# Performance work log

Hardware: AMD Instinct MI355X
Metric: run time of the kernel (lower is better)

The kernel has to match this reference:

```python
import jax, jax.numpy as jnp
import numpy as np

COST_CLASS = 1.0
COST_MASK = 1.0
COST_DICE = 1.0


def setup_inputs() -> dict:
    key = jax.random.key(0)
    k1, k2, k3, k4 = jax.random.split(key, 4)
    B, Q, G, T, L = 16, 100, 16384, 50, 21
    masks_queries_logits = jax.random.normal(k1, (B, Q, G), dtype=jnp.float32)
    class_queries_logits = jax.random.normal(k2, (B, Q, L), dtype=jnp.float32)
    mask_labels = (jax.random.uniform(k3, (B, T, G)) < 0.1).astype(jnp.float32)
    class_labels = jax.random.randint(k4, (B, T), 0, L, dtype=jnp.int64)
    return {
        "masks_queries_logits": masks_queries_logits,
        "class_queries_logits": class_queries_logits,
        "mask_labels": mask_labels,
        "class_labels": class_labels,
    }


def reference(masks_queries_logits, class_queries_logits, mask_labels, class_labels):
    """Returns the [B, Q, T] Hungarian cost matrices (the GPU-side compute of the
    matcher). The scipy linear_sum_assignment step is CPU-side and excluded."""
    G = masks_queries_logits.shape[-1]
    L = class_queries_logits.shape[-1]

    # classification cost: -softmax(pred)[:, target_class]
    probs = jax.nn.softmax(class_queries_logits, axis=-1)          # [B,Q,L]
    onehot = jax.nn.one_hot(class_labels, L, dtype=probs.dtype)    # [B,T,L]
    cost_class = -jnp.einsum('bql,btl->bqt', probs, onehot)        # [B,Q,T]

    # pairwise sigmoid cross-entropy cost (BCE-with-logits vs target 1 / target 0)
    ce_pos = jax.nn.softplus(-masks_queries_logits)                # [B,Q,G]
    ce_neg = jax.nn.softplus(masks_queries_logits)                 # [B,Q,G]
    cost_mask = (jnp.einsum('bqg,btg->bqt', ce_pos, mask_labels)
                 + jnp.einsum('bqg,btg->bqt', ce_neg, 1.0 - mask_labels)) / G

    # pairwise dice cost
    sig = jax.nn.sigmoid(masks_queries_logits)                     # [B,Q,G]
    numerator = 2.0 * jnp.einsum('bqg,btg->bqt', sig, mask_labels)
    denominator = sig.sum(-1)[:, :, None] + mask_labels.sum(-1)[:, None, :]
    cost_dice = 1.0 - (numerator + 1.0) / (denominator + 1.0)

    return COST_MASK * cost_mask + COST_CLASS * cost_class + COST_DICE * cost_dice
```

## Files before the change

### kernel.cpp

```cpp
#include <hip/hip_runtime.h>
#include <stdint.h>

#define NB 16
#define NQ 100
#define QP 112
#define NG 16384
#define NT 50
#define TP 64
#define NL 21
#define GW 512

#define OFF_BITS  0u
#define SZ_BITS   (NB*TP*GW*4u)
#define OFF_MSUM  (OFF_BITS + SZ_BITS)
#define SZ_MSUM   (NB*TP*4u)
#define OFF_SSP   (OFF_MSUM + SZ_MSUM)
#define SZ_SSP    (NB*QP*4u)
#define OFF_SSG   (OFF_SSP + SZ_SSP)
#define OFF_DOTM  (OFF_SSG + SZ_SSP)
#define SZ_DOT    (NB*QP*TP*4u)
#define OFF_DOTS  (OFF_DOTM + SZ_DOT)
#define ZERO_OFF  OFF_SSP
#define ZERO_SZ   (SZ_SSP*2u + SZ_DOT*2u)

typedef __bf16 bf16x8 __attribute__((ext_vector_type(8)));
typedef float f32x4 __attribute__((ext_vector_type(4)));
union Frag { uint32_t u[4]; bf16x8 v; };

__device__ __forceinline__ uint32_t pack_bf16(float a, float b) {
  uint32_t ua = __float_as_uint(a), ub = __float_as_uint(b);
  ua = (ua + 0x7FFFu + ((ua >> 16) & 1u)) >> 16;
  ub = (ub + 0x7FFFu + ((ub >> 16) & 1u)) & 0xFFFF0000u;
  return ua | ub;
}

__global__ __launch_bounds__(256) void pack_kernel(
    const float* __restrict__ mask, uint32_t* __restrict__ bits,
    float* __restrict__ msum) {
  int blk = blockIdx.x;
  int b = blk >> 6, t = blk & 63;
  int tid = threadIdx.x;
  int lane = tid & 63, wv = tid >> 6;
  uint32_t* wrow = bits + (size_t)(b*TP + t) * GW;
  if (t < NT) {
    const float* src = mask + (size_t)(b*NT + t) * NG;
    __shared__ int partial[4];
    int cnt = 0;
    int wbase = wv * 4096;
    for (int it = 0; it < 64; ++it) {
      int gb = wbase + it * 64;
      float v = src[gb + lane];
      unsigned long long bal = __ballot(v > 0.5f);
      if (lane == 0) wrow[gb >> 5] = (uint32_t)bal;
      if (lane == 1) wrow[(gb >> 5) + 1] = (uint32_t)(bal >> 32);
      cnt += (int)__popcll(bal);
    }
    if (lane == 0) partial[wv] = cnt;
    __syncthreads();
    if (tid == 0)
      msum[b*TP + t] = (float)(partial[0] + partial[1] + partial[2] + partial[3]);
  } else {
    for (int i = tid; i < GW; i += 256) wrow[i] = 0u;
    if (tid == 0) msum[b*TP + t] = 0.f;
  }
}

__global__ __launch_bounds__(448) void main_kernel(
    const float* __restrict__ m, const uint32_t* __restrict__ bits,
    float* __restrict__ ssp, float* __restrict__ ssg,
    float* __restrict__ dotm, float* __restrict__ dotsg) {
  int b = blockIdx.x >> 4;
  int chunk = blockIdx.x & 15;
  int tid = threadIdx.x;
  int wv = tid >> 6, lane = tid & 63;
  int row16 = lane & 15, lg = lane >> 4;

  __shared__ uint32_t lbits[TP][33];
  for (int i = tid; i < TP * 32; i += 448) {
    int t = i >> 5, k = i & 31;
    lbits[t][k] = bits[(size_t)(b*TP + t) * GW + chunk*32 + k];
  }
  __syncthreads();

  int q0 = wv * 16;
  int qrow = q0 + row16; if (qrow > NQ - 1) qrow = NQ - 1;
  const float* arow = m + (size_t)(b*NQ + qrow) * NG + chunk*1024 + lg*8;

  f32x4 accm[4], accs[4];
#pragma unroll
  for (int nt = 0; nt < 4; ++nt) {
    accm[nt] = (f32x4)(0.f);
    accs[nt] = (f32x4)(0.f);
  }
  float sspacc = 0.f, ssgacc = 0.f;

  for (int ks = 0; ks < 32; ++ks) {
    const float4* p = (const float4*)(arow + ks*32);
    float4 v0 = p[0], v1 = p[1];
    float av[8] = {v0.x, v0.y, v0.z, v0.w, v1.x, v1.y, v1.z, v1.w};
    Frag mf, sf;
#pragma unroll
    for (int j = 0; j < 8; j += 2) {
      float x0 = av[j], x1 = av[j+1];
      float e0 = __expf(-fabsf(x0)), e1 = __expf(-fabsf(x1));
      float r0 = __builtin_amdgcn_rcpf(1.f + e0);
      float r1 = __builtin_amdgcn_rcpf(1.f + e1);
      float sg0 = (x0 >= 0.f) ? r0 : 1.f - r0;
      float sg1 = (x1 >= 0.f) ? r1 : 1.f - r1;
      float sp0 = fmaxf(x0, 0.f) + __logf(1.f + e0);
      float sp1 = fmaxf(x1, 0.f) + __logf(1.f + e1);
      sspacc += sp0 + sp1;
      ssgacc += sg0 + sg1;
      mf.u[j >> 1] = pack_bf16(x0, x1);
      sf.u[j >> 1] = pack_bf16(sg0, sg1);
    }
#pragma unroll
    for (int nt = 0; nt < 4; ++nt) {
      int t = nt*16 + row16;
      uint32_t w = lbits[t][ks];
      uint32_t byte = (w >> (lg * 8)) & 0xFFu;
      Frag bf;
#pragma unroll
      for (int j = 0; j < 4; ++j) {
        uint32_t lo = (byte >> (2*j)) & 1u, hi = (byte >> (2*j + 1)) & 1u;
        bf.u[j] = (lo ? 0x3F80u : 0u) | (hi ? 0x3F800000u : 0u);
      }
      accm[nt] = __builtin_amdgcn_mfma_f32_16x16x32_bf16(mf.v, bf.v, accm[nt], 0, 0, 0);
      accs[nt] = __builtin_amdgcn_mfma_f32_16x16x32_bf16(sf.v, bf.v, accs[nt], 0, 0, 0);
    }
  }

  sspacc += __shfl_xor(sspacc, 16); sspacc += __shfl_xor(sspacc, 32);
  ssgacc += __shfl_xor(ssgacc, 16); ssgacc += __shfl_xor(ssgacc, 32);
  if (lg == 0) {
    atomicAdd(&ssp[b*QP + q0 + row16], sspacc);
    atomicAdd(&ssg[b*QP + q0 + row16], ssgacc);
  }
#pragma unroll
  for (int nt = 0; nt < 4; ++nt) {
    int t = nt*16 + row16;
#pragma unroll
    for (int r = 0; r < 4; ++r) {
      int qq = q0 + lg*4 + r;
      atomicAdd(&dotm[(size_t)(b*QP + qq)*TP + t], accm[nt][r]);
      atomicAdd(&dotsg[(size_t)(b*QP + qq)*TP + t], accs[nt][r]);
    }
  }
}

__global__ __launch_bounds__(64) void finalize_kernel(
    const float* __restrict__ cls, const int* __restrict__ labels,
    const float* __restrict__ msum, const float* __restrict__ ssp,
    const float* __restrict__ ssg, const float* __restrict__ dotm,
    const float* __restrict__ dotsg, float* __restrict__ out) {
  int blk = blockIdx.x;
  int b = blk / NQ, q = blk % NQ;
  int lane = threadIdx.x;
  const float* lgt = cls + (size_t)(b*NQ + q) * NL;
  float v = (lane < NL) ? lgt[lane] : -1e30f;
  float mx = v;
  for (int s = 32; s; s >>= 1) mx = fmaxf(mx, __shfl_xor(mx, s));
  float e = (lane < NL) ? __expf(v - mx) : 0.f;
  float se = e;
  for (int s = 32; s; s >>= 1) se += __shfl_xor(se, s);

  if (lane < NT) {
    int lbl = labels[b*NT + lane];
    float p = __expf(lgt[lbl] - mx) / se;
    float s1 = ssp[b*QP + q];
    float sg = ssg[b*QP + q];
    float dm = dotm[(size_t)(b*QP + q)*TP + lane];
    float ds = dotsg[(size_t)(b*QP + q)*TP + lane];
    float cmask = (s1 - dm) * (1.f / (float)NG);
    float cdice = 1.f - (2.f*ds + 1.f) / (sg + msum[b*TP + lane] + 1.f);
    out[(size_t)(b*NQ + q)*NT + lane] = cmask - p + cdice;
  }
}

extern "C" void kernel_launch(void* const* d_in, const int* in_sizes, int n_in,
                              void* d_out, int out_size, void* d_ws, size_t ws_size,
                              hipStream_t stream) {
  const float* mq = (const float*)d_in[0];
  const float* cq = (const float*)d_in[1];
  const float* ml = (const float*)d_in[2];
  const int*   cl = (const int*)d_in[3];
  char* ws = (char*)d_ws;
  uint32_t* bits = (uint32_t*)(ws + OFF_BITS);
  float* msum = (float*)(ws + OFF_MSUM);
  float* ssp  = (float*)(ws + OFF_SSP);
  float* ssg  = (float*)(ws + OFF_SSG);
  float* dotm = (float*)(ws + OFF_DOTM);
  float* dotsg= (float*)(ws + OFF_DOTS);

  hipMemsetAsync(ws + ZERO_OFF, 0, ZERO_SZ, stream);
  pack_kernel<<<NB*TP, 256, 0, stream>>>(ml, bits, msum);
  main_kernel<<<NB*16, 448, 0, stream>>>(mq, bits, ssp, ssg, dotm, dotsg);
  finalize_kernel<<<NB*NQ, 64, 0, stream>>>(cq, cl, msum, ssp, ssg, dotm, dotsg, (float*)d_out);
}
```

Before: 249.7 us.

## Pre-pack mask labels as bf16 MFMA fragments and fold row sums into GEMM

Adds a v2 path, taken when the workspace is large enough. Target masks are pre-packed as bf16 tiles already in MFMA B-fragment layout, so the main kernel loads fragments directly instead of expanding bits in LDS. An all-ones padding target (t=63) makes the MFMA produce the per-query sum of sigmoid and logit. Softplus is rewritten algebraically as x + log(1+e^-x), which removes the abs/select work and the separate sigmoid-sum accumulator. The main kernel now runs many small 64-thread blocks over 512-point chunks. In exchange it writes and reads a 32 MB packed buffer instead of a 2 MB bitmask, and the unguarded exp(-x) may overflow for very negative logits.

```diff
diff --git a/kernel.cpp b/kernel.cpp
--- a/kernel.cpp
+++ b/kernel.cpp
@@ -10,19 +10,6 @@
 #define NL 21
 #define GW 512
 
-#define OFF_BITS  0u
-#define SZ_BITS   (NB*TP*GW*4u)
-#define OFF_MSUM  (OFF_BITS + SZ_BITS)
-#define SZ_MSUM   (NB*TP*4u)
-#define OFF_SSP   (OFF_MSUM + SZ_MSUM)
-#define SZ_SSP    (NB*QP*4u)
-#define OFF_SSG   (OFF_SSP + SZ_SSP)
-#define OFF_DOTM  (OFF_SSG + SZ_SSP)
-#define SZ_DOT    (NB*QP*TP*4u)
-#define OFF_DOTS  (OFF_DOTM + SZ_DOT)
-#define ZERO_OFF  OFF_SSP
-#define ZERO_SZ   (SZ_SSP*2u + SZ_DOT*2u)
-
 typedef __bf16 bf16x8 __attribute__((ext_vector_type(8)));
 typedef float f32x4 __attribute__((ext_vector_type(4)));
 union Frag { uint32_t u[4]; bf16x8 v; };
@@ -34,7 +21,156 @@
   return ua | ub;
 }
 
-__global__ __launch_bounds__(256) void pack_kernel(
+#define SZ_BP     ((size_t)NB*512*64*32*2)
+#define OFF_MSUM2 (SZ_BP)
+#define OFF_SSP2  (OFF_MSUM2 + NB*TP*4)
+#define OFF_DOTM2 (OFF_SSP2 + NB*QP*4)
+#define OFF_DOTS2 (OFF_DOTM2 + (size_t)NB*QP*TP*4)
+#define NEED_V2   (OFF_DOTS2 + (size_t)NB*QP*TP*4)
+#define ZERO2_OFF OFF_MSUM2
+#define ZERO2_SZ  (NEED_V2 - OFF_MSUM2)
+
+__global__ __launch_bounds__(64) void pack_v2(
+    const float* __restrict__ mask, uint32_t* __restrict__ bp,
+    float* __restrict__ msum) {
+  int blk = blockIdx.x;
+  int qtr = blk & 3, t = (blk >> 2) & 63, b = blk >> 8;
+  int lane = threadIdx.x;
+  uint32_t* dst = bp + (size_t)b * (512*64*16);
+  if (t < NT) {
+    const float* src = mask + ((size_t)(b*NT + t)) * NG + qtr*4096;
+    float cnt = 0.f;
+#pragma unroll 4
+    for (int it = 0; it < 16; ++it) {
+      int g = it*256 + lane*4;
+      float4 v = *(const float4*)(src + g);
+      cnt += v.x + v.y + v.z + v.w;
+      int gg = qtr*4096 + g;
+      uint32_t* w = dst + ((size_t)(gg >> 5) * 64 + t) * 16 + ((gg & 31) >> 1);
+      uint2 pk; pk.x = pack_bf16(v.x, v.y); pk.y = pack_bf16(v.z, v.w);
+      *(uint2*)w = pk;
+    }
+    cnt += __shfl_xor(cnt, 1);  cnt += __shfl_xor(cnt, 2);
+    cnt += __shfl_xor(cnt, 4);  cnt += __shfl_xor(cnt, 8);
+    cnt += __shfl_xor(cnt, 16); cnt += __shfl_xor(cnt, 32);
+    if (lane == 0) atomicAdd(&msum[b*TP + t], cnt);
+  } else {
+    uint32_t val = (t == 63) ? 0x3F803F80u : 0u;
+    for (int it = 0; it < 16; ++it) {
+      int gg = qtr*4096 + it*256 + lane*4;
+      uint32_t* w = dst + ((size_t)(gg >> 5) * 64 + t) * 16 + ((gg & 31) >> 1);
+      uint2 pk; pk.x = val; pk.y = val;
+      *(uint2*)w = pk;
+    }
+  }
+}
+
+__global__ __launch_bounds__(64) void main_v2(
+    const float* __restrict__ m, const char* __restrict__ bp,
+    float* __restrict__ ssp, float* __restrict__ dotm,
+    float* __restrict__ dotsg) {
+  int blk = blockIdx.x;
+  int chunk = blk & 31;
+  int qt = (blk >> 5) % 7;
+  int b = blk / 224;
+  int lane = threadIdx.x;
+  int row16 = lane & 15, lg = lane >> 4;
+  int q0 = qt * 16;
+  int qrow = q0 + row16; if (qrow > NQ-1) qrow = NQ-1;
+  const float* arow = m + (size_t)(b*NQ + qrow)*NG + chunk*512 + lg*8;
+  const char* bbase = bp + (size_t)b*2097152 + (size_t)chunk*65536
+                         + (row16*32 + lg*8)*2;
+
+  f32x4 accm[4], accs[4];
+#pragma unroll
+  for (int nt = 0; nt < 4; ++nt) { accm[nt] = (f32x4)(0.f); accs[nt] = (f32x4)(0.f); }
+  float sl = 0.f;
+
+#pragma unroll 2
+  for (int ks = 0; ks < 16; ++ks) {
+    const float4* p = (const float4*)(arow + ks*32);
+    float4 v0 = p[0], v1 = p[1];
+    float av[8] = {v0.x, v0.y, v0.z, v0.w, v1.x, v1.y, v1.z, v1.w};
+    Frag mf, sf;
+#pragma unroll
+    for (int j = 0; j < 8; j += 2) {
+      float x0 = av[j], x1 = av[j+1];
+      float e0 = __builtin_amdgcn_exp2f(x0 * -1.442695041f);
+      float e1 = __builtin_amdgcn_exp2f(x1 * -1.442695041f);
+      float u0 = 1.f + e0, u1 = 1.f + e1;
+      float r0 = __builtin_amdgcn_rcpf(u0), r1 = __builtin_amdgcn_rcpf(u1);
+      sl += __builtin_amdgcn_logf(u0) + __builtin_amdgcn_logf(u1);
+      mf.u[j >> 1] = pack_bf16(x0, x1);
+      sf.u[j >> 1] = pack_bf16(r0, r1);
+    }
+    const char* bk = bbase + ks*4096;
+#pragma unroll
+    for (int nt = 0; nt < 4; ++nt) {
+      bf16x8 bfrag = *(const bf16x8*)(bk + nt*1024);
+      accm[nt] = __builtin_amdgcn_mfma_f32_16x16x32_bf16(mf.v, bfrag, accm[nt], 0, 0, 0);
+      accs[nt] = __builtin_amdgcn_mfma_f32_16x16x32_bf16(sf.v, bfrag, accs[nt], 0, 0, 0);
+    }
+  }
+
+  sl += __shfl_xor(sl, 16); sl += __shfl_xor(sl, 32);
+  if (lg == 0) atomicAdd(&ssp[b*QP + q0 + row16], sl);
+
+#pragma unroll
+  for (int nt = 0; nt < 4; ++nt) {
+    int t = nt*16 + row16;
+#pragma unroll
+    for (int r = 0; r < 4; ++r) {
+      int qq = q0 + lg*4 + r;
+      atomicAdd(&dotm [(size_t)(b*QP + qq)*TP + t], accm[nt][r]);
+      atomicAdd(&dotsg[(size_t)(b*QP + qq)*TP + t], accs[nt][r]);
+    }
+  }
+}
+
+__global__ __launch_bounds__(64) void finalize_v2(
+    const float* __restrict__ cls, const int* __restrict__ labels,
+    const float* __restrict__ msum, const float* __restrict__ ssp,
+    const float* __restrict__ dotm, const float* __restrict__ dotsg,
+    float* __restrict__ out) {
+  int blk = blockIdx.x;
+  int b = blk / NQ, q = blk % NQ;
+  int lane = threadIdx.x;
+  const float* lgt = cls + (size_t)(b*NQ + q) * NL;
+  float v = (lane < NL) ? lgt[lane] : -1e30f;
+  float mx = v;
+  for (int s = 32; s; s >>= 1) mx = fmaxf(mx, __shfl_xor(mx, s));
+  float e = (lane < NL) ? __expf(v - mx) : 0.f;
+  float se = e;
+  for (int s = 32; s; s >>= 1) se += __shfl_xor(se, s);
+
+  if (lane < NT) {
+    int lbl = labels[b*NT + lane];
+    float p = __expf(lgt[lbl] - mx) / se;
+    size_t base = (size_t)(b*QP + q) * TP;
+    float s1 = dotm[base + 63] + 0.69314718056f * ssp[b*QP + q];
+    float sg = dotsg[base + 63];
+    float dm = dotm[base + lane];
+    float ds = dotsg[base + lane];
+    float cmask = (s1 - dm) * (1.f / (float)NG);
+    float cdice = 1.f - (2.f*ds + 1.f) / (sg + msum[b*TP + lane] + 1.f);
+    out[(size_t)(b*NQ + q)*NT + lane] = cmask - p + cdice;
+  }
+}
+
+#define OFF1_BITS  0u
+#define SZ1_BITS   (NB*TP*GW*4u)
+#define OFF1_MSUM  (OFF1_BITS + SZ1_BITS)
+#define SZ1_MSUM   (NB*TP*4u)
+#define OFF1_SSP   (OFF1_MSUM + SZ1_MSUM)
+#define SZ1_SSP    (NB*QP*4u)
+#define OFF1_SSG   (OFF1_SSP + SZ1_SSP)
+#define OFF1_DOTM  (OFF1_SSG + SZ1_SSP)
+#define SZ1_DOT    (NB*QP*TP*4u)
+#define OFF1_DOTS  (OFF1_DOTM + SZ1_DOT)
+#define ZERO1_OFF  OFF1_SSP
+#define ZERO1_SZ   (SZ1_SSP*2u + SZ1_DOT*2u)
+
+__global__ __launch_bounds__(256) void pack_v1(
     const float* __restrict__ mask, uint32_t* __restrict__ bits,
     float* __restrict__ msum) {
   int blk = blockIdx.x;
@@ -65,7 +201,7 @@
   }
 }
 
-__global__ __launch_bounds__(448) void main_kernel(
+__global__ __launch_bounds__(448) void main_v1(
     const float* __restrict__ m, const uint32_t* __restrict__ bits,
     float* __restrict__ ssp, float* __restrict__ ssg,
     float* __restrict__ dotm, float* __restrict__ dotsg) {
@@ -88,10 +224,7 @@
 
   f32x4 accm[4], accs[4];
 #pragma unroll
-  for (int nt = 0; nt < 4; ++nt) {
-    accm[nt] = (f32x4)(0.f);
-    accs[nt] = (f32x4)(0.f);
-  }
+  for (int nt = 0; nt < 4; ++nt) { accm[nt] = (f32x4)(0.f); accs[nt] = (f32x4)(0.f); }
   float sspacc = 0.f, ssgacc = 0.f;
 
   for (int ks = 0; ks < 32; ++ks) {
@@ -148,7 +281,7 @@
   }
 }
 
-__global__ __launch_bounds__(64) void finalize_kernel(
+__global__ __launch_bounds__(64) void finalize_v1(
     const float* __restrict__ cls, const int* __restrict__ labels,
     const float* __restrict__ msum, const float* __restrict__ ssp,
     const float* __restrict__ ssg, const float* __restrict__ dotm,
@@ -185,15 +318,27 @@
   const float* ml = (const float*)d_in[2];
   const int*   cl = (const int*)d_in[3];
   char* ws = (char*)d_ws;
-  uint32_t* bits = (uint32_t*)(ws + OFF_BITS);
-  float* msum = (float*)(ws + OFF_MSUM);
-  float* ssp  = (float*)(ws + OFF_SSP);
-  float* ssg  = (float*)(ws + OFF_SSG);
-  float* dotm = (float*)(ws + OFF_DOTM);
-  float* dotsg= (float*)(ws + OFF_DOTS);
-
-  hipMemsetAsync(ws + ZERO_OFF, 0, ZERO_SZ, stream);
-  pack_kernel<<<NB*TP, 256, 0, stream>>>(ml, bits, msum);
-  main_kernel<<<NB*16, 448, 0, stream>>>(mq, bits, ssp, ssg, dotm, dotsg);
-  finalize_kernel<<<NB*NQ, 64, 0, stream>>>(cq, cl, msum, ssp, ssg, dotm, dotsg, (float*)d_out);
-}
+
+  if (ws_size >= NEED_V2) {
+    uint32_t* bp  = (uint32_t*)(ws);
+    float* msum = (float*)(ws + OFF_MSUM2);
+    float* ssp  = (float*)(ws + OFF_SSP2);
+    float* dotm = (float*)(ws + OFF_DOTM2);
+    float* dotsg= (float*)(ws + OFF_DOTS2);
+    hipMemsetAsync(ws + ZERO2_OFF, 0, ZERO2_SZ, stream);
+    pack_v2<<<NB*64*4, 64, 0, stream>>>(ml, bp, msum);
+    main_v2<<<NB*7*32, 64, 0, stream>>>(mq, (const char*)bp, ssp, dotm, dotsg);
+    finalize_v2<<<NB*NQ, 64, 0, stream>>>(cq, cl, msum, ssp, dotm, dotsg, (float*)d_out);
+  } else {
+    uint32_t* bits = (uint32_t*)(ws + OFF1_BITS);
+    float* msum = (float*)(ws + OFF1_MSUM);
+    float* ssp  = (float*)(ws + OFF1_SSP);
+    float* ssg  = (float*)(ws + OFF1_SSG);
+    float* dotm = (float*)(ws + OFF1_DOTM);
+    float* dotsg= (float*)(ws + OFF1_DOTS);
+    hipMemsetAsync(ws + ZERO1_OFF, 0, ZERO1_SZ, stream);
+    pack_v1<<<NB*TP, 256, 0, stream>>>(ml, bits, msum);
+    main_v1<<<NB*16, 448, 0, stream>>>(mq, bits, ssp, ssg, dotm, dotsg);
+    finalize_v1<<<NB*NQ, 64, 0, stream>>>(cq, cl, msum, ssp, ssg, dotm, dotsg, (float*)d_out);
+  }
+}
```

Measured after the change: 226.2 us. -9.4%, faster.

## Fuse mask packing into main kernel and fold row sums into MFMA

Applied to the files above, without the earlier changes.

Removes the separate bit-packing kernel: each block now loads its mask slice directly as bf16 into shared memory, laid out in MFMA fragment order. An all-ones padding target column and a padding query row let the MFMAs produce the sigmoid and logit row sums and the mask column sums, so the separate reductions go away. Softplus is rewritten as log(1+exp(-x)) summed with a log2 intrinsic, and the grid moves to 1024 blocks with smaller G chunks. This trades an extra kernel launch and a packed-bits round trip for more atomics and reading the full fp32 masks per block, and the unclamped exp can overflow for very negative logits.

```diff
diff --git a/kernel.cpp b/kernel.cpp
--- a/kernel.cpp
+++ b/kernel.cpp
@@ -8,20 +8,15 @@
 #define NT 50
 #define TP 64
 #define NL 21
-#define GW 512
+#define CH 256
+#define NCHUNK (NG/CH)
 
-#define OFF_BITS  0u
-#define SZ_BITS   (NB*TP*GW*4u)
-#define OFF_MSUM  (OFF_BITS + SZ_BITS)
-#define SZ_MSUM   (NB*TP*4u)
-#define OFF_SSP   (OFF_MSUM + SZ_MSUM)
-#define SZ_SSP    (NB*QP*4u)
-#define OFF_SSG   (OFF_SSP + SZ_SSP)
-#define OFF_DOTM  (OFF_SSG + SZ_SSP)
-#define SZ_DOT    (NB*QP*TP*4u)
-#define OFF_DOTS  (OFF_DOTM + SZ_DOT)
-#define ZERO_OFF  OFF_SSP
-#define ZERO_SZ   (SZ_SSP*2u + SZ_DOT*2u)
+#define OFF_SSP  0u
+#define SZ_SSP   (NB*QP*4u)
+#define OFF_DOTM (OFF_SSP + SZ_SSP)
+#define SZ_DOT   ((size_t)NB*QP*TP*4u)
+#define OFF_DOTS (OFF_DOTM + SZ_DOT)
+#define ZERO_SZ  (OFF_DOTS + SZ_DOT)
 
 typedef __bf16 bf16x8 __attribute__((ext_vector_type(8)));
 typedef float f32x4 __attribute__((ext_vector_type(4)));
@@ -34,67 +29,66 @@
   return ua | ub;
 }
 
-__global__ __launch_bounds__(256) void pack_kernel(
-    const float* __restrict__ mask, uint32_t* __restrict__ bits,
-    float* __restrict__ msum) {
-  int blk = blockIdx.x;
-  int b = blk >> 6, t = blk & 63;
-  int tid = threadIdx.x;
-  int lane = tid & 63, wv = tid >> 6;
-  uint32_t* wrow = bits + (size_t)(b*TP + t) * GW;
-  if (t < NT) {
-    const float* src = mask + (size_t)(b*NT + t) * NG;
-    __shared__ int partial[4];
-    int cnt = 0;
-    int wbase = wv * 4096;
-    for (int it = 0; it < 64; ++it) {
-      int gb = wbase + it * 64;
-      float v = src[gb + lane];
-      unsigned long long bal = __ballot(v > 0.5f);
-      if (lane == 0) wrow[gb >> 5] = (uint32_t)bal;
-      if (lane == 1) wrow[(gb >> 5) + 1] = (uint32_t)(bal >> 32);
-      cnt += (int)__popcll(bal);
-    }
-    if (lane == 0) partial[wv] = cnt;
-    __syncthreads();
-    if (tid == 0)
-      msum[b*TP + t] = (float)(partial[0] + partial[1] + partial[2] + partial[3]);
-  } else {
-    for (int i = tid; i < GW; i += 256) wrow[i] = 0u;
-    if (tid == 0) msum[b*TP + t] = 0.f;
-  }
+__device__ __forceinline__ uint32_t cvtpk(float a, float b) {
+  uint32_t r;
+  asm("v_cvt_pk_bf16_f32 %0, %1, %2" : "=v"(r) : "v"(a), "v"(b));
+  return r;
 }
 
-__global__ __launch_bounds__(448) void main_kernel(
-    const float* __restrict__ m, const uint32_t* __restrict__ bits,
-    float* __restrict__ ssp, float* __restrict__ ssg,
-    float* __restrict__ dotm, float* __restrict__ dotsg) {
-  int b = blockIdx.x >> 4;
-  int chunk = blockIdx.x & 15;
+__global__ __launch_bounds__(448, 7) void fused_main(
+    const float* __restrict__ m, const float* __restrict__ mask,
+    float* __restrict__ ssp, float* __restrict__ dotm,
+    float* __restrict__ dots) {
+  __shared__ __align__(16) uint32_t bfr[8 * 4 * 64 * 4];
+  int blk = blockIdx.x;
+  int chunk = blk & (NCHUNK - 1), b = blk >> 6;
   int tid = threadIdx.x;
-  int wv = tid >> 6, lane = tid & 63;
-  int row16 = lane & 15, lg = lane >> 4;
 
-  __shared__ uint32_t lbits[TP][33];
-  for (int i = tid; i < TP * 32; i += 448) {
-    int t = i >> 5, k = i & 31;
-    lbits[t][k] = bits[(size_t)(b*TP + t) * GW + chunk*32 + k];
+  {
+    int sub = tid & 7, tb = tid >> 3;
+    uint2* U2 = (uint2*)bfr;
+    int half = sub & 1;
+    int lgs = sub >> 1;
+    for (int t = tb; t < 64; t += 56) {
+      int nt = t >> 4;
+      int l = lgs * 16 + (t & 15);
+      if (t < NT) {
+        const float* src = mask + ((size_t)(b*NT + t))*NG + chunk*CH + sub*4;
+#pragma unroll
+        for (int i = 0; i < 8; ++i) {
+          float4 f = *(const float4*)(src + i*32);
+          uint2 pk;
+          pk.x = pack_bf16(f.x, f.y);
+          pk.y = pack_bf16(f.z, f.w);
+          U2[((i*4 + nt)*64 + l)*2 + half] = pk;
+        }
+      } else {
+        uint32_t c = (t == 63) ? 0x3F803F80u : 0u;
+        uint2 pk; pk.x = c; pk.y = c;
+#pragma unroll
+        for (int i = 0; i < 8; ++i)
+          U2[((i*4 + nt)*64 + l)*2 + half] = pk;
+      }
+    }
   }
   __syncthreads();
 
+  int lane = tid & 63, wv = tid >> 6;
+  int row16 = lane & 15, lg = lane >> 4;
   int q0 = wv * 16;
-  int qrow = q0 + row16; if (qrow > NQ - 1) qrow = NQ - 1;
-  const float* arow = m + (size_t)(b*NQ + qrow) * NG + chunk*1024 + lg*8;
+  int qrow = q0 + row16;
+  bool pad = qrow > NQ - 1;
+  int qc = pad ? NQ - 1 : qrow;
+  const float* arow = m + (size_t)(b*NQ + qc)*NG + chunk*CH + lg*8;
+  const bf16x8* BF = (const bf16x8*)bfr;
 
   f32x4 accm[4], accs[4];
 #pragma unroll
-  for (int nt = 0; nt < 4; ++nt) {
-    accm[nt] = (f32x4)(0.f);
-    accs[nt] = (f32x4)(0.f);
-  }
-  float sspacc = 0.f, ssgacc = 0.f;
+  for (int nt = 0; nt < 4; ++nt) { accm[nt] = (f32x4)(0.f); accs[nt] = (f32x4)(0.f); }
+  float sl = 0.f;
 
-  for (int ks = 0; ks < 32; ++ks) {
+#pragma unroll 2
+  for (int ks = 0; ks < 8; ++ks) {
     const float4* p = (const float4*)(arow + ks*32);
     float4 v0 = p[0], v1 = p[1];
     float av[8] = {v0.x, v0.y, v0.z, v0.w, v1.x, v1.y, v1.z, v1.w};
@@ -102,40 +96,27 @@
 #pragma unroll
     for (int j = 0; j < 8; j += 2) {
       float x0 = av[j], x1 = av[j+1];
-      float e0 = __expf(-fabsf(x0)), e1 = __expf(-fabsf(x1));
-      float r0 = __builtin_amdgcn_rcpf(1.f + e0);
-      float r1 = __builtin_amdgcn_rcpf(1.f + e1);
-      float sg0 = (x0 >= 0.f) ? r0 : 1.f - r0;
-      float sg1 = (x1 >= 0.f) ? r1 : 1.f - r1;
-      float sp0 = fmaxf(x0, 0.f) + __logf(1.f + e0);
-      float sp1 = fmaxf(x1, 0.f) + __logf(1.f + e1);
-      sspacc += sp0 + sp1;
-      ssgacc += sg0 + sg1;
-      mf.u[j >> 1] = pack_bf16(x0, x1);
-      sf.u[j >> 1] = pack_bf16(sg0, sg1);
+      x0 = pad ? 1.f : x0;
+      x1 = pad ? 1.f : x1;
+      float e0 = __builtin_amdgcn_exp2f(x0 * -1.442695041f);
+      float e1 = __builtin_amdgcn_exp2f(x1 * -1.442695041f);
+      float u0 = 1.f + e0, u1 = 1.f + e1;
+      float r0 = __builtin_amdgcn_rcpf(u0), r1 = __builtin_amdgcn_rcpf(u1);
+      sl += __builtin_amdgcn_logf(u0) + __builtin_amdgcn_logf(u1);
+      mf.u[j >> 1] = cvtpk(x0, x1);
+      sf.u[j >> 1] = cvtpk(r0, r1);
     }
 #pragma unroll
     for (int nt = 0; nt < 4; ++nt) {
-      int t = nt*16 + row16;
-      uint32_t w = lbits[t][ks];
-      uint32_t byte = (w >> (lg * 8)) & 0xFFu;
-      Frag bf;
-#pragma unroll
-      for (int j = 0; j < 4; ++j) {
-        uint32_t lo = (byte >> (2*j)) & 1u, hi = (byte >> (2*j + 1)) & 1u;
-        bf.u[j] = (lo ? 0x3F80u : 0u) | (hi ? 0x3F800000u : 0u);
-      }
-      accm[nt] = __builtin_amdgcn_mfma_f32_16x16x32_bf16(mf.v, bf.v, accm[nt], 0, 0, 0);
-      accs[nt] = __builtin_amdgcn_mfma_f32_16x16x32_bf16(sf.v, bf.v, accs[nt], 0, 0, 0);
+      bf16x8 bb = BF[(ks*4 + nt)*64 + lane];
+      accm[nt] = __builtin_amdgcn_mfma_f32_16x16x32_bf16(mf.v, bb, accm[nt], 0, 0, 0);
+      accs[nt] = __builtin_amdgcn_mfma_f32_16x16x32_bf16(sf.v, bb, accs[nt], 0, 0, 0);
     }
   }
 
-  sspacc += __shfl_xor(sspacc, 16); sspacc += __shfl_xor(sspacc, 32);
-  ssgacc += __shfl_xor(ssgacc, 16); ssgacc += __shfl_xor(ssgacc, 32);
-  if (lg == 0) {
-    atomicAdd(&ssp[b*QP + q0 + row16], sspacc);
-    atomicAdd(&ssg[b*QP + q0 + row16], ssgacc);
-  }
+  sl += __shfl_xor(sl, 16); sl += __shfl_xor(sl, 32);
+  if (lg == 0) atomicAdd(&ssp[b*QP + q0 + row16], sl);
+
 #pragma unroll
   for (int nt = 0; nt < 4; ++nt) {
     int t = nt*16 + row16;
@@ -143,16 +124,15 @@
     for (int r = 0; r < 4; ++r) {
       int qq = q0 + lg*4 + r;
       atomicAdd(&dotm[(size_t)(b*QP + qq)*TP + t], accm[nt][r]);
-      atomicAdd(&dotsg[(size_t)(b*QP + qq)*TP + t], accs[nt][r]);
+      atomicAdd(&dots[(size_t)(b*QP + qq)*TP + t], accs[nt][r]);
     }
   }
 }
 
-__global__ __launch_bounds__(64) void finalize_kernel(
+__global__ __launch_bounds__(64) void finalize_k(
     const float* __restrict__ cls, const int* __restrict__ labels,
-    const float* __restrict__ msum, const float* __restrict__ ssp,
-    const float* __restrict__ ssg, const float* __restrict__ dotm,
-    const float* __restrict__ dotsg, float* __restrict__ out) {
+    const float* __restrict__ ssp, const float* __restrict__ dotm,
+    const float* __restrict__ dots, float* __restrict__ out) {
   int blk = blockIdx.x;
   int b = blk / NQ, q = blk % NQ;
   int lane = threadIdx.x;
@@ -167,12 +147,14 @@
   if (lane < NT) {
     int lbl = labels[b*NT + lane];
     float p = __expf(lgt[lbl] - mx) / se;
-    float s1 = ssp[b*QP + q];
-    float sg = ssg[b*QP + q];
-    float dm = dotm[(size_t)(b*QP + q)*TP + lane];
-    float ds = dotsg[(size_t)(b*QP + q)*TP + lane];
+    size_t base = (size_t)(b*QP + q) * TP;
+    float s1 = dotm[base + 63] + 0.69314718056f * ssp[b*QP + q];
+    float sg = dots[base + 63];
+    float msum = dotm[(size_t)(b*QP + 111)*TP + lane];
+    float dm = dotm[base + lane];
+    float ds = dots[base + lane];
     float cmask = (s1 - dm) * (1.f / (float)NG);
-    float cdice = 1.f - (2.f*ds + 1.f) / (sg + msum[b*TP + lane] + 1.f);
+    float cdice = 1.f - (2.f*ds + 1.f) / (sg + msum + 1.f);
     out[(size_t)(b*NQ + q)*NT + lane] = cmask - p + cdice;
   }
 }
@@ -185,15 +167,11 @@
   const float* ml = (const float*)d_in[2];
   const int*   cl = (const int*)d_in[3];
   char* ws = (char*)d_ws;
-  uint32_t* bits = (uint32_t*)(ws + OFF_BITS);
-  float* msum = (float*)(ws + OFF_MSUM);
   float* ssp  = (float*)(ws + OFF_SSP);
-  float* ssg  = (float*)(ws + OFF_SSG);
   float* dotm = (float*)(ws + OFF_DOTM);
-  float* dotsg= (float*)(ws + OFF_DOTS);
+  float* dots = (float*)(ws + OFF_DOTS);
 
-  hipMemsetAsync(ws + ZERO_OFF, 0, ZERO_SZ, stream);
-  pack_kernel<<<NB*TP, 256, 0, stream>>>(ml, bits, msum);
-  main_kernel<<<NB*16, 448, 0, stream>>>(mq, bits, ssp, ssg, dotm, dotsg);
-  finalize_kernel<<<NB*NQ, 64, 0, stream>>>(cq, cl, msum, ssp, ssg, dotm, dotsg, (float*)d_out);
+  hipMemsetAsync(ws, 0, ZERO_SZ, stream);
+  fused_main<<<NB*NCHUNK, 448, 0, stream>>>(mq, ml, ssp, dotm, dots);
+  finalize_k<<<NB*NQ, 64, 0, stream>>>(cq, cl, ssp, dotm, dots, (float*)d_out);
 }
```

Measured after the change: 225.4 us. 1.11x faster.
